# Kernel optimization log

Measured on AMD Instinct MI355X. Metric: run time of the kernel, lower is better.

The kernel has to match this reference:

```python
import jax, jax.numpy as jnp
import numpy as np

N = 10000       # nodes
E = 320000      # edges (before self-loops)
IN = 128
HID = 256
OUT = 256
HEADS = 4
C = HID // HEADS  # 64 per-head channels
NEG_SLOPE = 0.2   # PyG GATConv default
BN_EPS = 1e-5


def setup_inputs() -> dict:
    key = jax.random.key(0)
    ks = jax.random.split(key, 24)
    x = jax.random.normal(ks[0], (N, IN), jnp.float32)
    edge_index = jax.random.randint(ks[1], (2, E), 0, N, dtype=jnp.int64)

    def glorot(k, shape, fan_in):
        return jax.random.normal(k, shape, jnp.float32) * (1.0 / np.sqrt(fan_in))

    inp = {"x": x, "edge_index": edge_index}
    # layer 0: IN -> HEADS x C (concat)
    inp["W0"] = glorot(ks[2], (IN, HEADS * C), IN)
    inp["as0"] = glorot(ks[3], (HEADS, C), C)
    inp["ad0"] = glorot(ks[4], (HEADS, C), C)
    inp["b0"] = jnp.zeros((HEADS * C,), jnp.float32)
    inp["g0"] = jnp.ones((HID,), jnp.float32)
    inp["be0"] = jnp.zeros((HID,), jnp.float32)
    # layer 1: HID -> HEADS x C (concat)
    inp["W1"] = glorot(ks[5], (HID, HEADS * C), HID)
    inp["as1"] = glorot(ks[6], (HEADS, C), C)
    inp["ad1"] = glorot(ks[7], (HEADS, C), C)
    inp["b1"] = jnp.zeros((HEADS * C,), jnp.float32)
    inp["g1"] = jnp.ones((HID,), jnp.float32)
    inp["be1"] = jnp.zeros((HID,), jnp.float32)
    # layer 2: HID -> OUT, heads=1, concat=False
    inp["W2"] = glorot(ks[8], (HID, OUT), HID)
    inp["as2"] = glorot(ks[9], (1, OUT), OUT)
    inp["ad2"] = glorot(ks[10], (1, OUT), OUT)
    inp["b2"] = jnp.zeros((OUT,), jnp.float32)
    inp["g2"] = jnp.ones((OUT,), jnp.float32)
    inp["be2"] = jnp.zeros((OUT,), jnp.float32)
    return inp


def gat_conv(x, src, dst, W, att_src, att_dst, bias, concat):
    """PyG GATConv (add_self_loops already applied to src/dst)."""
    H, Ch = att_src.shape
    h = (x @ W).reshape(-1, H, Ch)                      # [N, H, C]
    a_src = jnp.einsum('nhc,hc->nh', h, att_src)        # [N, H]
    a_dst = jnp.einsum('nhc,hc->nh', h, att_dst)
    alpha = jax.nn.leaky_relu(a_src[src] + a_dst[dst], NEG_SLOPE)  # [E', H]
    # segment softmax over incoming edges of each dst node
    amax = jax.ops.segment_max(alpha, dst, num_segments=N)
    alpha = jnp.exp(alpha - amax[dst])
    denom = jax.ops.segment_sum(alpha, dst, num_segments=N)
    alpha = alpha / (denom[dst] + 1e-16)
    msg = h[src] * alpha[:, :, None]                    # [E', H, C]
    out = jax.ops.segment_sum(msg, dst, num_segments=N) # [N, H, C]
    out = out.reshape(N, H * Ch) if concat else out.mean(axis=1)
    return out + bias


def batch_norm(x, gamma, beta):
    # training-mode BatchNorm1d over node dim (biased variance, eps=1e-5)
    m = x.mean(axis=0)
    v = jnp.mean((x - m) ** 2, axis=0)
    return (x - m) * jax.lax.rsqrt(v + BN_EPS) * gamma + beta


def reference(x, edge_index,
              W0, as0, ad0, b0, g0, be0,
              W1, as1, ad1, b1, g1, be1,
              W2, as2, ad2, b2, g2, be2):
    loop = jnp.arange(N, dtype=edge_index.dtype)
    src = jnp.concatenate([edge_index[0], loop])
    dst = jnp.concatenate([edge_index[1], loop])

    h = gat_conv(x, src, dst, W0, as0, ad0, b0, concat=True)
    h = jax.nn.relu(batch_norm(h, g0, be0))  # dropout inactive in eval
    h = gat_conv(h, src, dst, W1, as1, ad1, b1, concat=True)
    h = jax.nn.relu(batch_norm(h, g1, be1))
    h = gat_conv(h, src, dst, W2, as2, ad2, b2, concat=False)
    h = batch_norm(h, g2, be2)
    return h
```

## Files before the change

### kernel.cpp

```cpp
#include <hip/hip_runtime.h>
#include <math.h>

#define NN 10000
#define EE 320000
#define ET (EE + NN)

typedef __attribute__((ext_vector_type(8))) short short8;
typedef __attribute__((ext_vector_type(8))) unsigned short ushort8_t;
typedef __attribute__((ext_vector_type(4))) float f32x4;
typedef unsigned short u16;

static __device__ __forceinline__ float b2f(u16 u) {
  return __uint_as_float(((unsigned)u) << 16);
}
static __device__ __forceinline__ u16 f2b(float f) {
  unsigned u = __float_as_uint(f);
  unsigned r = (u + 0x7FFFu + ((u >> 16) & 1u)) >> 16;
  return (u16)r;
}

__global__ void k_castcnt(const int* __restrict__ ei, int* __restrict__ cnt,
                          const float* __restrict__ x, const float* __restrict__ W0,
                          const float* __restrict__ W1, const float* __restrict__ W2,
                          u16* __restrict__ abf, u16* __restrict__ Wt0,
                          u16* __restrict__ Wt1, u16* __restrict__ Wt2) {
  int t = blockIdx.x * 256 + threadIdx.x;
  if (t < EE) atomicAdd(&cnt[ei[EE + t]], 1);
  const int NX4 = NN * 128 / 4;
  if (t < NX4) {
    float4 f = ((const float4*)x)[t];
    ushort4 o;
    o.x = f2b(f.x); o.y = f2b(f.y); o.z = f2b(f.z); o.w = f2b(f.w);
    ((ushort4*)abf)[t] = o;
    return;
  }
  int u = t - NX4;
  if (u < 128 * 256) {
    int nI = u / 128, k = u - nI * 128;
    Wt0[u] = f2b(W0[(size_t)k * 256 + nI]);
    return;
  }
  u -= 128 * 256;
  if (u < 256 * 256) {
    int nI = u / 256, k = u - nI * 256;
    Wt1[u] = f2b(W1[(size_t)k * 256 + nI]);
    return;
  }
  u -= 256 * 256;
  if (u < 256 * 256) {
    int nI = u / 256, k = u - nI * 256;
    Wt2[u] = f2b(W2[(size_t)k * 256 + nI]);
  }
}

__global__ __launch_bounds__(1024) void k_scan(const int* __restrict__ cnt,
                                               int* __restrict__ rowst,
                                               int* __restrict__ cursor,
                                               int* __restrict__ csrc) {
  __shared__ int ws[16];
  int tid = threadIdx.x, lane = tid & 63, wv = tid >> 6;
  int base = tid * 10;
  int v[10];
  int tot = 0;
#pragma unroll
  for (int i = 0; i < 10; i++) {
    int idx = base + i;
    v[i] = (idx < NN) ? (cnt[idx] + 1) : 0;
    tot += v[i];
  }
  int sc = tot;
#pragma unroll
  for (int off = 1; off < 64; off <<= 1) {
    int t = __shfl_up(sc, off);
    if (lane >= off) sc += t;
  }
  if (lane == 63) ws[wv] = sc;
  __syncthreads();
  if (wv == 0 && lane < 16) {
    int val = ws[lane];
    int s = val;
#pragma unroll
    for (int off = 1; off < 16; off <<= 1) {
      int t = __shfl_up(s, off);
      if (lane >= off) s += t;
    }
    ws[lane] = s - val;
  }
  __syncthreads();
  int run = ws[wv] + sc - tot;
#pragma unroll
  for (int i = 0; i < 10; i++) {
    int idx = base + i;
    if (idx < NN) {
      rowst[idx] = run;
      csrc[run] = idx;
      cursor[idx] = run + 1;
      run += v[i];
    }
  }
  if (tid == 1023) rowst[NN] = run;
}

__global__ void k_fill(const int* __restrict__ ei, int* __restrict__ cursor,
                       int* __restrict__ csrc) {
  int e = blockIdx.x * 256 + threadIdx.x;
  if (e < EE) {
    int d = ei[EE + e];
    int pos = atomicAdd(&cursor[d], 1);
    csrc[pos] = ei[e];
  }
}

template <int KK, int BN>
__global__ __launch_bounds__(256) void k_gemm(
    const u16* __restrict__ A, const float* __restrict__ bkt,
    const float* __restrict__ gam, const float* __restrict__ bet,
    const u16* __restrict__ Wt, const float* __restrict__ as,
    const float* __restrict__ ad, u16* __restrict__ hb,
    float* __restrict__ asrc, float* __restrict__ adst, int H) {
  __shared__ float2 bnp[256];
  if (BN) {
    int t = threadIdx.x;
    float s = 0.f, q = 0.f;
#pragma unroll 8
    for (int b = 0; b < 32; b++) {
      s += bkt[b * 512 + t];
      q += bkt[b * 512 + 256 + t];
    }
    float m = s * (1.0f / NN);
    float v = q * (1.0f / NN) - m * m;
    float rs = rsqrtf(v + 1e-5f) * gam[t];
    bnp[t] = make_float2(rs, bet[t] - m * rs);
    __syncthreads();
  }
  int wv = threadIdx.x >> 6, lane = threadIdx.x & 63;
  int row0 = blockIdx.x * 64 + wv * 16;
  int col0 = blockIdx.y * 128;
  int r = lane & 15, g = lane >> 4;
  f32x4 acc[8];
#pragma unroll
  for (int nt = 0; nt < 8; nt++) acc[nt] = (f32x4){0.f, 0.f, 0.f, 0.f};

  int ar = row0 + r;
  if (ar > NN - 1) ar = NN - 1;

#pragma unroll
  for (int ks = 0; ks < KK / 32; ks++) {
    short8 af;
    short8 raw = *(const short8*)(A + (size_t)ar * KK + ks * 32 + g * 8);
    if (BN == 0) {
      af = raw;
    } else {
      int c0 = ks * 32 + g * 8;
#pragma unroll
      for (int j = 0; j < 8; j++) {
        float2 p = bnp[c0 + j];
        float t = fmaxf(fmaf(b2f((u16)raw[j]), p.x, p.y), 0.f);
        af[j] = (short)f2b(t);
      }
    }
#pragma unroll
    for (int nt = 0; nt < 8; nt++) {
      short8 bf = *(const short8*)(Wt + (size_t)(col0 + nt * 16 + r) * KK + ks * 32 + g * 8);
      acc[nt] = __builtin_amdgcn_mfma_f32_16x16x32_bf16(af, bf, acc[nt], 0, 0, 0);
    }
  }
#pragma unroll
  for (int nt = 0; nt < 8; nt++) {
    int col = col0 + nt * 16 + r;
#pragma unroll
    for (int q = 0; q < 4; q++) {
      int row = row0 + g * 4 + q;
      if (row < NN) hb[(size_t)row * 256 + col] = f2b(acc[nt][q]);
    }
  }
  float asv[8], adv[8];
#pragma unroll
  for (int nt = 0; nt < 8; nt++) {
    asv[nt] = as[col0 + nt * 16 + r];
    adv[nt] = ad[col0 + nt * 16 + r];
  }
#pragma unroll
  for (int q = 0; q < 4; q++) {
    int row = row0 + g * 4 + q;
    if (H == 4) {
#pragma unroll
      for (int hh = 0; hh < 2; hh++) {
        float ps = 0.f, pd = 0.f;
#pragma unroll
        for (int k = 0; k < 4; k++) {
          ps = fmaf(acc[hh * 4 + k][q], asv[hh * 4 + k], ps);
          pd = fmaf(acc[hh * 4 + k][q], adv[hh * 4 + k], pd);
        }
#pragma unroll
        for (int off = 1; off < 16; off <<= 1) {
          ps += __shfl_xor(ps, off);
          pd += __shfl_xor(pd, off);
        }
        if (r == 0 && row < NN) {
          int slot = 2 * blockIdx.y + hh;
          asrc[row * 4 + slot] = ps;
          adst[row * 4 + slot] = pd;
        }
      }
    } else {
      float ps = 0.f, pd = 0.f;
#pragma unroll
      for (int nt = 0; nt < 8; nt++) {
        ps = fmaf(acc[nt][q], asv[nt], ps);
        pd = fmaf(acc[nt][q], adv[nt], pd);
      }
#pragma unroll
      for (int off = 1; off < 16; off <<= 1) {
        ps += __shfl_xor(ps, off);
        pd += __shfl_xor(pd, off);
      }
      if (r == 0 && row < NN) {
        int slot = 2 * blockIdx.y;
        asrc[row * 4 + slot] = ps;
        asrc[row * 4 + slot + 1] = 0.f;
        adst[row * 4 + slot] = pd;
        adst[row * 4 + slot + 1] = 0.f;
      }
    }
  }
}

template <int H, int BOUT>
__global__ __launch_bounds__(256) void k_softagg(
    const int* __restrict__ rowst, const int* __restrict__ csrc,
    const float* __restrict__ asrc, const float* __restrict__ adst,
    const u16* __restrict__ hb, const float* __restrict__ bias,
    float* __restrict__ outf, u16* __restrict__ outb, float* __restrict__ bkt) {
  __shared__ int lds_s[4][128];
  __shared__ float lds_w[4][128][H];
  __shared__ float lds_v[4][256];
  __shared__ float lds_q[4][256];
  int wv = threadIdx.x >> 6, lane = threadIdx.x & 63;
  int n = blockIdx.x * 4 + wv;
  int rs = rowst[n], re = rowst[n + 1];

  float ad[H];
  {
    float4 t = ((const float4*)adst)[n];
    if (H == 4) { ad[0] = t.x; ad[1] = t.y; ad[2] = t.z; ad[3] = t.w; }
    else ad[0] = t.x + t.y + t.z + t.w;
  }
  float mx[H], sm[H];
#pragma unroll
  for (int h = 0; h < H; h++) { mx[h] = -1e30f; sm[h] = 0.f; }

  int e0 = rs + lane, e1 = e0 + 64;
  bool h0 = e0 < re, h1 = e1 < re;
  float a0[H], a1[H];

  if (h0) {
    int s = csrc[e0];
    lds_s[wv][lane] = s;
    float4 t = ((const float4*)asrc)[s];
    if (H == 4) { a0[0] = t.x; a0[1] = t.y; a0[2] = t.z; a0[3] = t.w; }
    else a0[0] = t.x + t.y + t.z + t.w;
#pragma unroll
    for (int h = 0; h < H; h++) {
      float v = a0[h] + ad[h];
      v = v > 0.f ? v : 0.2f * v;
      a0[h] = v;
      mx[h] = fmaxf(mx[h], v);
    }
  }
  if (h1) {
    int s = csrc[e1];
    lds_s[wv][64 + lane] = s;
    float4 t = ((const float4*)asrc)[s];
    if (H == 4) { a1[0] = t.x; a1[1] = t.y; a1[2] = t.z; a1[3] = t.w; }
    else a1[0] = t.x + t.y + t.z + t.w;
#pragma unroll
    for (int h = 0; h < H; h++) {
      float v = a1[h] + ad[h];
      v = v > 0.f ? v : 0.2f * v;
      a1[h] = v;
      mx[h] = fmaxf(mx[h], v);
    }
  }
  for (int e = rs + 128 + lane; e < re; e += 64) {
    int s = csrc[e];
    float4 t = ((const float4*)asrc)[s];
    float a[H];
    if (H == 4) { a[0] = t.x; a[1] = t.y; a[2] = t.z; a[3] = t.w; }
    else a[0] = t.x + t.y + t.z + t.w;
#pragma unroll
    for (int h = 0; h < H; h++) {
      float v = a[h] + ad[h];
      v = v > 0.f ? v : 0.2f * v;
      mx[h] = fmaxf(mx[h], v);
    }
  }
#pragma unroll
  for (int off = 32; off; off >>= 1)
#pragma unroll
    for (int h = 0; h < H; h++) mx[h] = fmaxf(mx[h], __shfl_xor(mx[h], off));

  if (h0) {
#pragma unroll
    for (int h = 0; h < H; h++) {
      a0[h] = __expf(a0[h] - mx[h]);
      sm[h] += a0[h];
      lds_w[wv][lane][h] = a0[h];
    }
  }
  if (h1) {
#pragma unroll
    for (int h = 0; h < H; h++) {
      a1[h] = __expf(a1[h] - mx[h]);
      sm[h] += a1[h];
      lds_w[wv][64 + lane][h] = a1[h];
    }
  }
  for (int e = rs + 128 + lane; e < re; e += 64) {
    int s = csrc[e];
    float4 t = ((const float4*)asrc)[s];
    float a[H];
    if (H == 4) { a[0] = t.x; a[1] = t.y; a[2] = t.z; a[3] = t.w; }
    else a[0] = t.x + t.y + t.z + t.w;
#pragma unroll
    for (int h = 0; h < H; h++) {
      float v = a[h] + ad[h];
      v = v > 0.f ? v : 0.2f * v;
      sm[h] += __expf(v - mx[h]);
    }
  }
#pragma unroll
  for (int off = 32; off; off >>= 1)
#pragma unroll
    for (int h = 0; h < H; h++) sm[h] += __shfl_xor(sm[h], off);

  float inv[H];
#pragma unroll
  for (int h = 0; h < H; h++) inv[h] = 1.0f / (sm[h] + 1e-16f);

  int m = re - rs;
  if (m > 128) m = 128;
  int mp = (m + 15) & ~15;
  for (int p = m + lane; p < mp; p += 64) {
    lds_s[wv][p] = n;
#pragma unroll
    for (int h = 0; h < H; h++) lds_w[wv][p][h] = 0.f;
  }

  int cl = lane & 31, half = lane >> 5;
  int hd8 = (H == 4) ? (cl >> 3) : 0;
  float invh = (H == 4) ? (hd8 == 0 ? inv[0] : hd8 == 1 ? inv[1] : hd8 == 2 ? inv[2] : inv[3])
                        : inv[0];
  float mh = (H == 4) ? (hd8 == 0 ? mx[0] : hd8 == 1 ? mx[1] : hd8 == 2 ? mx[2] : mx[3])
                      : mx[0];
  float adh = (H == 4) ? (hd8 == 0 ? ad[0] : hd8 == 1 ? ad[1] : hd8 == 2 ? ad[2] : ad[3])
                       : ad[0];
  const ushort8_t* h8 = (const ushort8_t*)hb;
  float acc[8] = {0.f, 0.f, 0.f, 0.f, 0.f, 0.f, 0.f, 0.f};
  for (int e = 0; e < mp; e += 16) {
    int ss[8];
    float ww[8];
    ushort8_t vv[8];
#pragma unroll
    for (int j = 0; j < 8; j++) ss[j] = lds_s[wv][e + 2 * j + half];
#pragma unroll
    for (int j = 0; j < 8; j++) ww[j] = lds_w[wv][e + 2 * j + half][hd8];
#pragma unroll
    for (int j = 0; j < 8; j++) vv[j] = h8[(size_t)ss[j] * 32 + cl];
#pragma unroll
    for (int j = 0; j < 8; j++)
#pragma unroll
      for (int k = 0; k < 8; k++) acc[k] = fmaf(ww[j], b2f((u16)vv[j][k]), acc[k]);
  }
  for (int ee = rs + 128 + half; ee < re; ee += 2) {
    int s = csrc[ee];
    float4 t = ((const float4*)asrc)[s];
    float av = (H == 4) ? (hd8 == 0 ? t.x : hd8 == 1 ? t.y : hd8 == 2 ? t.z : t.w)
                        : (t.x + t.y + t.z + t.w);
    float vv2 = av + adh;
    vv2 = vv2 > 0.f ? vv2 : 0.2f * vv2;
    float w = __expf(vv2 - mh);
    ushort8_t v = h8[(size_t)s * 32 + cl];
#pragma unroll
    for (int k = 0; k < 8; k++) acc[k] = fmaf(w, b2f((u16)v[k]), acc[k]);
  }
#pragma unroll
  for (int k = 0; k < 8; k++) acc[k] += __shfl_xor(acc[k], 32);

  float4 ba = ((const float4*)bias)[cl * 2];
  float4 bb = ((const float4*)bias)[cl * 2 + 1];
  float r8[8];
  r8[0] = acc[0] * invh + ba.x; r8[1] = acc[1] * invh + ba.y;
  r8[2] = acc[2] * invh + ba.z; r8[3] = acc[3] * invh + ba.w;
  r8[4] = acc[4] * invh + bb.x; r8[5] = acc[5] * invh + bb.y;
  r8[6] = acc[6] * invh + bb.z; r8[7] = acc[7] * invh + bb.w;

  if (half == 0) {
    if (BOUT) {
      ushort8_t o;
#pragma unroll
      for (int k = 0; k < 8; k++) o[k] = f2b(r8[k]);
      ((ushort8_t*)outb)[(size_t)n * 32 + cl] = o;
    } else {
      float4 w0 = make_float4(r8[0], r8[1], r8[2], r8[3]);
      float4 w1 = make_float4(r8[4], r8[5], r8[6], r8[7]);
      ((float4*)outf)[(size_t)n * 64 + cl * 2] = w0;
      ((float4*)outf)[(size_t)n * 64 + cl * 2 + 1] = w1;
    }
#pragma unroll
    for (int k = 0; k < 8; k++) {
      lds_v[wv][cl * 8 + k] = r8[k];
      lds_q[wv][cl * 8 + k] = r8[k] * r8[k];
    }
  }
  __syncthreads();
  int t = threadIdx.x;
  float sv = lds_v[0][t] + lds_v[1][t] + lds_v[2][t] + lds_v[3][t];
  float sq = lds_q[0][t] + lds_q[1][t] + lds_q[2][t] + lds_q[3][t];
  float* pv = bkt + (blockIdx.x & 31) * 512;
  atomicAdd(pv + t, sv);
  atomicAdd(pv + 256 + t, sq);
}

__global__ void k_bnred(const float* __restrict__ bkt, const float* __restrict__ g,
                        const float* __restrict__ be, float* __restrict__ rsg,
                        float* __restrict__ sh) {
  int t = threadIdx.x;
  float s = 0.f, q = 0.f;
#pragma unroll 8
  for (int b = 0; b < 32; b++) {
    s += bkt[b * 512 + t];
    q += bkt[b * 512 + 256 + t];
  }
  float m = s * (1.0f / NN);
  float v = q * (1.0f / NN) - m * m;
  float rs = rsqrtf(v + 1e-5f) * g[t];
  rsg[t] = rs;
  sh[t] = be[t] - m * rs;
}

__global__ void k_bnout(const float* __restrict__ x, const float* __restrict__ rsg,
                        const float* __restrict__ sh, float* __restrict__ y) {
  int i = blockIdx.x * 256 + threadIdx.x;
  int c = i & 63;
  float4 rs4 = ((const float4*)rsg)[c];
  float4 sh4 = ((const float4*)sh)[c];
  float4 xv = ((const float4*)x)[i];
  float4 r;
  r.x = fmaf(xv.x, rs4.x, sh4.x);
  r.y = fmaf(xv.y, rs4.y, sh4.y);
  r.z = fmaf(xv.z, rs4.z, sh4.z);
  r.w = fmaf(xv.w, rs4.w, sh4.w);
  ((float4*)y)[i] = r;
}

extern "C" void kernel_launch(void* const* d_in, const int* in_sizes, int n_in,
                              void* d_out, int out_size, void* d_ws, size_t ws_size,
                              hipStream_t stream) {
  const float* x   = (const float*)d_in[0];
  const int*   ei  = (const int*)d_in[1];
  const float* W0  = (const float*)d_in[2];
  const float* as0 = (const float*)d_in[3];
  const float* ad0 = (const float*)d_in[4];
  const float* b0  = (const float*)d_in[5];
  const float* g0  = (const float*)d_in[6];
  const float* be0 = (const float*)d_in[7];
  const float* W1  = (const float*)d_in[8];
  const float* as1 = (const float*)d_in[9];
  const float* ad1 = (const float*)d_in[10];
  const float* b1  = (const float*)d_in[11];
  const float* g1  = (const float*)d_in[12];
  const float* be1 = (const float*)d_in[13];
  const float* W2  = (const float*)d_in[14];
  const float* as2 = (const float*)d_in[15];
  const float* ad2 = (const float*)d_in[16];
  const float* b2  = (const float*)d_in[17];
  const float* g2  = (const float*)d_in[18];
  const float* be2 = (const float*)d_in[19];
  float* out = (float*)d_out;

  u16* hb   = (u16*)d_ws;
  u16* abf  = hb + (size_t)NN * 256;
  u16* ab16 = abf + (size_t)NN * 128;
  u16* Wt0  = ab16 + (size_t)NN * 256;
  u16* Wt1  = Wt0 + 256 * 128;
  u16* Wt2  = Wt1 + 256 * 256;
  float* asrc = (float*)(Wt2 + 256 * 256);
  float* adst = asrc + NN * 4;
  float* aggf = adst + NN * 4;
  float* bkt  = aggf + (size_t)NN * 256;
  float* rsg2 = bkt + 3 * 32 * 512;
  float* sh2  = rsg2 + 256;
  int* cnt    = (int*)(sh2 + 256);
  int* rowst  = cnt + NN;
  int* cursor = rowst + NN + 1;
  int* csrc   = cursor + NN;

  hipMemsetAsync(bkt, 0, (3 * 32 * 512 + 512 + NN) * sizeof(float), stream);
  {
    int total = NN * 128 / 4 + 128 * 256 + 256 * 256 + 256 * 256;
    k_castcnt<<<(total + 255) / 256, 256, 0, stream>>>(ei, cnt, x, W0, W1, W2,
                                                       abf, Wt0, Wt1, Wt2);
  }
  k_scan<<<1, 1024, 0, stream>>>(cnt, rowst, cursor, csrc);
  k_fill<<<(EE + 255) / 256, 256, 0, stream>>>(ei, cursor, csrc);

  dim3 ggrid((NN + 63) / 64, 2);

  k_gemm<128, 0><<<ggrid, 256, 0, stream>>>(abf, nullptr, nullptr, nullptr,
                                            Wt0, as0, ad0, hb, asrc, adst, 4);
  k_softagg<4, 1><<<NN / 4, 256, 0, stream>>>(rowst, csrc, asrc, adst, hb, b0,
                                              nullptr, ab16, bkt);

  k_gemm<256, 1><<<ggrid, 256, 0, stream>>>(ab16, bkt, g0, be0,
                                            Wt1, as1, ad1, hb, asrc, adst, 4);
  k_softagg<4, 1><<<NN / 4, 256, 0, stream>>>(rowst, csrc, asrc, adst, hb, b1,
                                              nullptr, ab16, bkt + 32 * 512);

  k_gemm<256, 1><<<ggrid, 256, 0, stream>>>(ab16, bkt + 32 * 512, g1, be1,
                                            Wt2, as2, ad2, hb, asrc, adst, 1);
  k_softagg<1, 0><<<NN / 4, 256, 0, stream>>>(rowst, csrc, asrc, adst, hb, b2,
                                              aggf, nullptr, bkt + 2 * 32 * 512);

  k_bnred<<<1, 256, 0, stream>>>(bkt + 2 * 32 * 512, g2, be2, rsg2, sh2);
  k_bnout<<<NN / 4, 256, 0, stream>>>(aggf, rsg2, sh2, out);
}
```

Baseline: 293.1 us.

## Fuse CSR fill into first GEMM, tile weight transpose, stage GEMM stores via LDS

The CSR fill work runs as extra blocks of the first GEMM launch instead of its own kernel. The BN-parameter reduction is folded into the output normalisation kernel, so two launches disappear. Weight transposes now go through a padded shared-memory tile to coalesce reads and writes. GEMM outputs are staged in LDS and written as 16-byte vectors, and hb is padded to 10048 rows so edge tiles can store without a bounds check. Each BN-out block recomputes the 256 statistics redundantly, and fill blocks now share the GEMM launch.

```diff
diff --git a/kernel.cpp b/kernel.cpp
--- a/kernel.cpp
+++ b/kernel.cpp
@@ -4,6 +4,7 @@
 #define NN 10000
 #define EE 320000
 #define ET (EE + NN)
+#define HBROWS 10048
 
 typedef __attribute__((ext_vector_type(8))) short short8;
 typedef __attribute__((ext_vector_type(8))) unsigned short ushort8_t;
@@ -19,37 +20,39 @@
   return (u16)r;
 }
 
-__global__ void k_castcnt(const int* __restrict__ ei, int* __restrict__ cnt,
-                          const float* __restrict__ x, const float* __restrict__ W0,
-                          const float* __restrict__ W1, const float* __restrict__ W2,
-                          u16* __restrict__ abf, u16* __restrict__ Wt0,
-                          u16* __restrict__ Wt1, u16* __restrict__ Wt2) {
-  int t = blockIdx.x * 256 + threadIdx.x;
-  if (t < EE) atomicAdd(&cnt[ei[EE + t]], 1);
-  const int NX4 = NN * 128 / 4;
-  if (t < NX4) {
-    float4 f = ((const float4*)x)[t];
+__global__ __launch_bounds__(256) void k_castcnt(
+    const int* __restrict__ ei, int* __restrict__ cnt, const float* __restrict__ x,
+    const float* __restrict__ W0, const float* __restrict__ W1,
+    const float* __restrict__ W2, u16* __restrict__ abf, u16* __restrict__ Wt0,
+    u16* __restrict__ Wt1, u16* __restrict__ Wt2) {
+  int b = blockIdx.x, tid = threadIdx.x;
+  if (b < 1250) {
+    int e = b * 256 + tid;
+    atomicAdd(&cnt[ei[EE + e]], 1);
+    float4 f = ((const float4*)x)[e];
     ushort4 o;
     o.x = f2b(f.x); o.y = f2b(f.y); o.z = f2b(f.z); o.w = f2b(f.w);
-    ((ushort4*)abf)[t] = o;
+    ((ushort4*)abf)[e] = o;
     return;
   }
-  int u = t - NX4;
-  if (u < 128 * 256) {
-    int nI = u / 128, k = u - nI * 128;
-    Wt0[u] = f2b(W0[(size_t)k * 256 + nI]);
-    return;
-  }
-  u -= 128 * 256;
-  if (u < 256 * 256) {
-    int nI = u / 256, k = u - nI * 256;
-    Wt1[u] = f2b(W1[(size_t)k * 256 + nI]);
-    return;
-  }
-  u -= 256 * 256;
-  if (u < 256 * 256) {
-    int nI = u / 256, k = u - nI * 256;
-    Wt2[u] = f2b(W2[(size_t)k * 256 + nI]);
+  __shared__ float tile[64][65];
+  int wt = b - 1250;
+  const float* W; u16* Wt; int K, kt, nt_;
+  if (wt < 8)       { W = W0; Wt = Wt0; K = 128; kt = wt & 1; nt_ = wt >> 1; }
+  else if (wt < 24) { W = W1; Wt = Wt1; K = 256; int u = wt - 8;  kt = u & 3; nt_ = u >> 2; }
+  else              { W = W2; Wt = Wt2; K = 256; int u = wt - 24; kt = u & 3; nt_ = u >> 2; }
+  int k0 = kt * 64, n0 = nt_ * 64;
+  int tx = tid & 63, ty = tid >> 6;
+#pragma unroll
+  for (int it = 0; it < 16; it++) {
+    int row = it * 4 + ty;
+    tile[row][tx] = W[(size_t)(k0 + row) * 256 + n0 + tx];
+  }
+  __syncthreads();
+#pragma unroll
+  for (int it = 0; it < 16; it++) {
+    int row = it * 4 + ty;
+    Wt[(size_t)(n0 + row) * K + k0 + tx] = f2b(tile[tx][row]);
   }
 }
 
@@ -101,24 +104,25 @@
   if (tid == 1023) rowst[NN] = run;
 }
 
-__global__ void k_fill(const int* __restrict__ ei, int* __restrict__ cursor,
-                       int* __restrict__ csrc) {
-  int e = blockIdx.x * 256 + threadIdx.x;
-  if (e < EE) {
-    int d = ei[EE + e];
-    int pos = atomicAdd(&cursor[d], 1);
-    csrc[pos] = ei[e];
-  }
-}
-
-template <int KK, int BN>
+template <int KK, int BN, int FILL>
 __global__ __launch_bounds__(256) void k_gemm(
     const u16* __restrict__ A, const float* __restrict__ bkt,
     const float* __restrict__ gam, const float* __restrict__ bet,
     const u16* __restrict__ Wt, const float* __restrict__ as,
     const float* __restrict__ ad, u16* __restrict__ hb,
-    float* __restrict__ asrc, float* __restrict__ adst, int H) {
+    float* __restrict__ asrc, float* __restrict__ adst, int H,
+    const int* __restrict__ ei, int* __restrict__ cursor, int* __restrict__ csrc) {
+  if (FILL && blockIdx.x >= 314) {
+    int e = (blockIdx.x - 314) * 256 + threadIdx.x;
+    if (e < EE) {
+      int d = ei[EE + e];
+      int pos = atomicAdd(&cursor[d], 1);
+      csrc[pos] = ei[e];
+    }
+    return;
+  }
   __shared__ float2 bnp[256];
+  __shared__ u16 lds_c[4][16][136];
   if (BN) {
     int t = threadIdx.x;
     float s = 0.f, q = 0.f;
@@ -134,8 +138,9 @@
     __syncthreads();
   }
   int wv = threadIdx.x >> 6, lane = threadIdx.x & 63;
-  int row0 = blockIdx.x * 64 + wv * 16;
-  int col0 = blockIdx.y * 128;
+  int gx = blockIdx.x >> 1, gy = blockIdx.x & 1;
+  int row0 = gx * 64 + wv * 16;
+  int col0 = gy * 128;
   int r = lane & 15, g = lane >> 4;
   f32x4 acc[8];
 #pragma unroll
@@ -166,13 +171,16 @@
     }
   }
 #pragma unroll
-  for (int nt = 0; nt < 8; nt++) {
-    int col = col0 + nt * 16 + r;
-#pragma unroll
-    for (int q = 0; q < 4; q++) {
-      int row = row0 + g * 4 + q;
-      if (row < NN) hb[(size_t)row * 256 + col] = f2b(acc[nt][q]);
-    }
+  for (int nt = 0; nt < 8; nt++)
+#pragma unroll
+    for (int q = 0; q < 4; q++)
+      lds_c[wv][g * 4 + q][nt * 16 + r] = f2b(acc[nt][q]);
+#pragma unroll
+  for (int j = 0; j < 4; j++) {
+    int c = j * 64 + lane;
+    int row = c >> 4, off = (c & 15) * 8;
+    ushort8_t vv = *(const ushort8_t*)&lds_c[wv][row][off];
+    *(ushort8_t*)&hb[(size_t)(row0 + row) * 256 + col0 + off] = vv;
   }
   float asv[8], adv[8];
 #pragma unroll
@@ -198,7 +206,7 @@
           pd += __shfl_xor(pd, off);
         }
         if (r == 0 && row < NN) {
-          int slot = 2 * blockIdx.y + hh;
+          int slot = 2 * gy + hh;
           asrc[row * 4 + slot] = ps;
           adst[row * 4 + slot] = pd;
         }
@@ -216,7 +224,7 @@
         pd += __shfl_xor(pd, off);
       }
       if (r == 0 && row < NN) {
-        int slot = 2 * blockIdx.y;
+        int slot = 2 * gy;
         asrc[row * 4 + slot] = ps;
         asrc[row * 4 + slot + 1] = 0.f;
         adst[row * 4 + slot] = pd;
@@ -422,9 +430,12 @@
   atomicAdd(pv + 256 + t, sq);
 }
 
-__global__ void k_bnred(const float* __restrict__ bkt, const float* __restrict__ g,
-                        const float* __restrict__ be, float* __restrict__ rsg,
-                        float* __restrict__ sh) {
+__global__ __launch_bounds__(256) void k_bnout(const float* __restrict__ bkt,
+                                               const float* __restrict__ g,
+                                               const float* __restrict__ be,
+                                               const float* __restrict__ x,
+                                               float* __restrict__ y) {
+  __shared__ float2 p[256];
   int t = threadIdx.x;
   float s = 0.f, q = 0.f;
 #pragma unroll 8
@@ -435,22 +446,17 @@
   float m = s * (1.0f / NN);
   float v = q * (1.0f / NN) - m * m;
   float rs = rsqrtf(v + 1e-5f) * g[t];
-  rsg[t] = rs;
-  sh[t] = be[t] - m * rs;
-}
-
-__global__ void k_bnout(const float* __restrict__ x, const float* __restrict__ rsg,
-                        const float* __restrict__ sh, float* __restrict__ y) {
-  int i = blockIdx.x * 256 + threadIdx.x;
+  p[t] = make_float2(rs, be[t] - m * rs);
+  __syncthreads();
+  int i = blockIdx.x * 256 + t;
   int c = i & 63;
-  float4 rs4 = ((const float4*)rsg)[c];
-  float4 sh4 = ((const float4*)sh)[c];
+  float2 p0 = p[c * 4], p1 = p[c * 4 + 1], p2 = p[c * 4 + 2], p3 = p[c * 4 + 3];
   float4 xv = ((const float4*)x)[i];
   float4 r;
-  r.x = fmaf(xv.x, rs4.x, sh4.x);
-  r.y = fmaf(xv.y, rs4.y, sh4.y);
-  r.z = fmaf(xv.z, rs4.z, sh4.z);
-  r.w = fmaf(xv.w, rs4.w, sh4.w);
+  r.x = fmaf(xv.x, p0.x, p0.y);
+  r.y = fmaf(xv.y, p1.x, p1.y);
+  r.z = fmaf(xv.z, p2.x, p2.y);
+  r.w = fmaf(xv.w, p3.x, p3.y);
   ((float4*)y)[i] = r;
 }
 
@@ -480,7 +486,7 @@
   float* out = (float*)d_out;
 
   u16* hb   = (u16*)d_ws;
-  u16* abf  = hb + (size_t)NN * 256;
+  u16* abf  = hb + (size_t)HBROWS * 256;
   u16* ab16 = abf + (size_t)NN * 128;
   u16* Wt0  = ab16 + (size_t)NN * 256;
   u16* Wt1  = Wt0 + 256 * 128;
@@ -489,39 +495,32 @@
   float* adst = asrc + NN * 4;
   float* aggf = adst + NN * 4;
   float* bkt  = aggf + (size_t)NN * 256;
-  float* rsg2 = bkt + 3 * 32 * 512;
-  float* sh2  = rsg2 + 256;
-  int* cnt    = (int*)(sh2 + 256);
+  int* cnt    = (int*)(bkt + 3 * 32 * 512);
   int* rowst  = cnt + NN;
   int* cursor = rowst + NN + 1;
   int* csrc   = cursor + NN;
 
-  hipMemsetAsync(bkt, 0, (3 * 32 * 512 + 512 + NN) * sizeof(float), stream);
-  {
-    int total = NN * 128 / 4 + 128 * 256 + 256 * 256 + 256 * 256;
-    k_castcnt<<<(total + 255) / 256, 256, 0, stream>>>(ei, cnt, x, W0, W1, W2,
-                                                       abf, Wt0, Wt1, Wt2);
-  }
+  hipMemsetAsync(bkt, 0, (3 * 32 * 512 + NN) * sizeof(float), stream);
+  k_castcnt<<<1290, 256, 0, stream>>>(ei, cnt, x, W0, W1, W2, abf, Wt0, Wt1, Wt2);
   k_scan<<<1, 1024, 0, stream>>>(cnt, rowst, cursor, csrc);
-  k_fill<<<(EE + 255) / 256, 256, 0, stream>>>(ei, cursor, csrc);
-
-  dim3 ggrid((NN + 63) / 64, 2);
-
-  k_gemm<128, 0><<<ggrid, 256, 0, stream>>>(abf, nullptr, nullptr, nullptr,
-                                            Wt0, as0, ad0, hb, asrc, adst, 4);
+
+  k_gemm<128, 0, 1><<<314 + 1250, 256, 0, stream>>>(
+      abf, nullptr, nullptr, nullptr, Wt0, as0, ad0, hb, asrc, adst, 4,
+      ei, cursor, csrc);
   k_softagg<4, 1><<<NN / 4, 256, 0, stream>>>(rowst, csrc, asrc, adst, hb, b0,
                                               nullptr, ab16, bkt);
 
-  k_gemm<256, 1><<<ggrid, 256, 0, stream>>>(ab16, bkt, g0, be0,
-                                            Wt1, as1, ad1, hb, asrc, adst, 4);
+  k_gemm<256, 1, 0><<<314, 256, 0, stream>>>(
+      ab16, bkt, g0, be0, Wt1, as1, ad1, hb, asrc, adst, 4,
+      nullptr, nullptr, nullptr);
   k_softagg<4, 1><<<NN / 4, 256, 0, stream>>>(rowst, csrc, asrc, adst, hb, b1,
                                               nullptr, ab16, bkt + 32 * 512);
 
-  k_gemm<256, 1><<<ggrid, 256, 0, stream>>>(ab16, bkt + 32 * 512, g1, be1,
-                                            Wt2, as2, ad2, hb, asrc, adst, 1);
+  k_gemm<256, 1, 0><<<314, 256, 0, stream>>>(
+      ab16, bkt + 32 * 512, g1, be1, Wt2, as2, ad2, hb, asrc, adst, 1,
+      nullptr, nullptr, nullptr);
   k_softagg<1, 0><<<NN / 4, 256, 0, stream>>>(rowst, csrc, asrc, adst, hb, b2,
                                               aggf, nullptr, bkt + 2 * 32 * 512);
 
-  k_bnred<<<1, 256, 0, stream>>>(bkt + 2 * 32 * 512, g2, be2, rsg2, sh2);
-  k_bnout<<<NN / 4, 256, 0, stream>>>(aggf, rsg2, sh2, out);
-}
+  k_bnout<<<NN / 4, 256, 0, stream>>>(bkt + 2 * 32 * 512, g2, be2, aggf, out);
+}
```

Measured after the change: 281.8 us (median of 2 runs). 3.8% less time.
